# Kernel tuning notes

Measured on AMD Instinct MI355X. Metric: run time of the kernel, lower is better.

## Reference

```python
import jax, jax.numpy as jnp
import numpy as np

B = 2048        # batch
FEAT = 2048     # backbone feature dim (NIMA_attr stub input)
NUM_BINS = 9    # must match len(arange(1,5.5,0.5))
NUM_ATTR = 12
NUM_PT = 20
D = 64          # input_dim
H = 256         # hidden_size


def _mlp(x, W1, b1, W2, b2):
    return jax.nn.relu(x @ W1 + b1) @ W2 + b2


def _internal_interaction(e, W1, b1, W2, b2):
    # e: [B, A, D]; pairwise elementwise products -> tiny MLP -> sum over first attr axis
    pair = e[:, :, None, :] * e[:, None, :, :]          # [B, A, A, D]
    return _mlp(pair, W1, b1, W2, b2).sum(axis=1)       # [B, A, D]


def _gru_step(x, h, Wih, Whh, bih, bhh):
    # PyTorch GRUCell math; Wih/Whh stored as [D, 3D] with gate order r,z,n
    gi = x @ Wih + bih
    gh = h @ Whh + bhh
    ir, iz, inn = jnp.split(gi, 3, axis=-1)
    hr, hz, hn = jnp.split(gh, 3, axis=-1)
    r = jax.nn.sigmoid(ir + hr)
    z = jax.nn.sigmoid(iz + hz)
    n = jnp.tanh(inn + r * hn)
    return (1.0 - z) * n + z * h


def _interfuse(init, internal, external, Wih, Whh, bih, bhh):
    # so we batch the attribute dim and run the 3 sequential GRU steps once.
    h = _gru_step(init, jnp.zeros_like(init), Wih, Whh, bih, bhh)
    h = _gru_step(internal, h, Wih, Whh, bih, bhh)
    h = _gru_step(external, h, Wih, Whh, bih, bhh)
    return h


def setup_inputs() -> dict:
    key = jax.random.key(0)
    ks = jax.random.split(key, 40)
    def p(i, shape):
        return jax.random.normal(ks[i], shape, dtype=jnp.float32) * 0.05
    return dict(
        images=jax.random.normal(ks[0], (B, FEAT), dtype=jnp.float32),
        personal_traits=jax.random.normal(ks[1], (B, NUM_PT), dtype=jnp.float32),
        nima_Wl=p(2, (FEAT, NUM_BINS)), nima_bl=p(3, (NUM_BINS,)),
        nima_Wa=p(4, (FEAT, NUM_ATTR)), nima_ba=p(5, (NUM_ATTR,)),
        img_node_W1=p(6, (NUM_ATTR, H)), img_node_b1=p(7, (H,)),
        img_node_W2=p(8, (H, NUM_ATTR * D)), img_node_b2=p(9, (NUM_ATTR * D,)),
        user_node_W1=p(10, (NUM_PT, H)), user_node_b1=p(11, (H,)),
        user_node_W2=p(12, (H, NUM_ATTR * D)), user_node_b2=p(13, (NUM_ATTR * D,)),
        ii_img_W1=p(14, (D, H)), ii_img_b1=p(15, (H,)),
        ii_img_W2=p(16, (H, D)), ii_img_b2=p(17, (D,)),
        ii_user_W1=p(18, (D, H)), ii_user_b1=p(19, (H,)),
        ii_user_W2=p(20, (H, D)), ii_user_b2=p(21, (D,)),
        gru_img_Wih=p(22, (D, 3 * D)), gru_img_Whh=p(23, (D, 3 * D)),
        gru_img_bih=p(24, (3 * D,)), gru_img_bhh=p(25, (3 * D,)),
        gru_user_Wih=p(26, (D, 3 * D)), gru_user_Whh=p(27, (D, 3 * D)),
        gru_user_bih=p(28, (3 * D,)), gru_user_bhh=p(29, (3 * D,)),
        corr_W=p(30, (D, 1)), corr_b=p(31, (1,)),
        dist_W1=p(32, (NUM_BINS, H)), dist_b1=p(33, (H,)),
        dist_W2=p(34, (H, 1)), dist_b2=p(35, (1,)),
    )


def reference(images, personal_traits,
              nima_Wl, nima_bl, nima_Wa, nima_ba,
              img_node_W1, img_node_b1, img_node_W2, img_node_b2,
              user_node_W1, user_node_b1, user_node_W2, user_node_b2,
              ii_img_W1, ii_img_b1, ii_img_W2, ii_img_b2,
              ii_user_W1, ii_user_b1, ii_user_W2, ii_user_b2,
              gru_img_Wih, gru_img_Whh, gru_img_bih, gru_img_bhh,
              gru_user_Wih, gru_user_Whh, gru_user_bih, gru_user_bhh,
              corr_W, corr_b, dist_W1, dist_b1, dist_W2, dist_b2):
    # NIMA_attr stub: two linear heads on backbone features
    logit = images @ nima_Wl + nima_bl                       # [B, num_bins]
    attr_raw = images @ nima_Wa + nima_ba                    # [B, num_attr]

    attr_img = _mlp(attr_raw, img_node_W1, img_node_b1, img_node_W2, img_node_b2)
    attr_img = attr_img.reshape(-1, NUM_ATTR, D)
    attr_user = _mlp(personal_traits, user_node_W1, user_node_b1, user_node_W2, user_node_b2)
    attr_user = attr_user.reshape(-1, NUM_ATTR, D)

    prob = jax.nn.softmax(logit, axis=1)

    internal_img = _internal_interaction(attr_img, ii_img_W1, ii_img_b1, ii_img_W2, ii_img_b2)
    internal_user = _internal_interaction(attr_user, ii_user_W1, ii_user_b1, ii_user_W2, ii_user_b2)

    # ExternalInteraction: interaction[:,i,j] = user_i * img_j; sums factor out
    ext_user = attr_user * attr_img.sum(axis=1, keepdims=True)   # sum over j
    ext_img = attr_img * attr_user.sum(axis=1, keepdims=True)    # sum over i

    fused_img = _interfuse(attr_img, internal_img, ext_img,
                           gru_img_Wih, gru_img_Whh, gru_img_bih, gru_img_bhh)
    fused_user = _interfuse(attr_user, internal_user, ext_user,
                            gru_user_Wih, gru_user_Whh, gru_user_bih, gru_user_bhh)

    interaction_outputs = (fused_img.sum(axis=1) + fused_user.sum(axis=1)) @ corr_W + corr_b

    scale = jnp.arange(NUM_BINS, dtype=jnp.float32) * 0.5 + 1.0   # arange(1,5.5,0.5)
    direct_outputs = _mlp(prob * scale, dist_W1, dist_b1, dist_W2, dist_b2)
    return interaction_outputs + direct_outputs                  # [B, 1]
```

## Files before the change

kernel.cpp:

```cpp
#include <hip/hip_runtime.h>
#include <hip/hip_bf16.h>

#define NB 2048
#define FEAT 2048
#define NBINS 9
#define NATTR 12
#define NPT 20
#define DD 64
#define HH 256

typedef __attribute__((ext_vector_type(8))) short bf8v;
typedef __attribute__((ext_vector_type(4))) float f4v;
typedef __attribute__((ext_vector_type(16))) float f16v;

__device__ __forceinline__ unsigned short f2bf(float f) {
  unsigned int u = __float_as_uint(f);
  u += 0x7FFFu + ((u >> 16) & 1u);
  return (unsigned short)(u >> 16);
}

__device__ __forceinline__ unsigned int pkbf(float x, float y) {
  __hip_bfloat162 h = __float22bfloat162_rn(make_float2(x, y));
  union { __hip_bfloat162 h; unsigned int u; } cv;
  cv.h = h;
  return cv.u;
}

__global__ void k_prep_all(
    const float* __restrict__ Wl, const float* __restrict__ Wa,
    const float* __restrict__ Wih_i, const float* __restrict__ Whh_i,
    const float* __restrict__ Wih_u, const float* __restrict__ Whh_u,
    const float* __restrict__ W1i, const float* __restrict__ W1u,
    const float* __restrict__ W2i, const float* __restrict__ W2u,
    float* __restrict__ WT, unsigned short* __restrict__ WTg,
    unsigned short* __restrict__ W1T, unsigned short* __restrict__ W2T,
    float* __restrict__ outacc) {
  int bid = blockIdx.x, tid = threadIdx.x;
  if (bid < 168) {
    int idx = bid * 256 + tid;
    if (idx < 21 * FEAT) {
      int c = idx / FEAT, k = idx - c * FEAT;
      WT[idx] = (c < NBINS) ? Wl[k * NBINS + c] : Wa[k * NATTR + (c - NBINS)];
    }
  } else if (bid < 172) {
    if (tid < 192) {
      int idx = bid - 168;
      const float* W = idx == 0 ? Wih_i : idx == 1 ? Whh_i : idx == 2 ? Wih_u : Whh_u;
      unsigned short* dst = WTg + (size_t)idx * 192 * 72 + (size_t)tid * 72;
      for (int k = 0; k < DD; ++k) dst[k] = f2bf(W[k * 192 + tid]);
    }
  } else if (bid < 428) {
    int t = (bid - 172) * 256 + tid;
    if (t < 32768) {
      int dt = t >> 14, rem = t & 16383;
      int h = rem >> 6, k = rem & 63;
      W1T[t] = f2bf((dt ? W1u : W1i)[k * HH + h]);
    } else {
      int t2 = t - 32768;
      int dt = t2 >> 14, rem = t2 & 16383;
      int dp = rem >> 8, k = rem & 255;
      W2T[t2] = f2bf((dt ? W2u : W2i)[k * DD + dp]);
    }
  } else {
    int idx = (bid - 428) * 256 + tid;
    if (idx < NB) outacc[idx] = 0.f;
  }
}

__global__ __launch_bounds__(256) void k_nima(
    const float* __restrict__ A, const float* __restrict__ WT,
    const float* __restrict__ bl, const float* __restrict__ ba,
    const float* __restrict__ dW1, const float* __restrict__ db1,
    const float* __restrict__ dW2, const float* __restrict__ db2,
    float* __restrict__ attr_raw, float* __restrict__ direct) {
  int wave = threadIdx.x >> 6, lane = threadIdx.x & 63;
  int row = blockIdx.x * 4 + wave;
  const float4* A4 = (const float4*)(A + (size_t)row * FEAT);
  float acc[21];
#pragma unroll
  for (int c = 0; c < 21; ++c) acc[c] = 0.f;
#pragma unroll
  for (int it = 0; it < 8; ++it) {
    int kk = it * 64 + lane;
    float4 a = A4[kk];
#pragma unroll
    for (int c = 0; c < 21; ++c) {
      float4 w = ((const float4*)(WT + c * FEAT))[kk];
      acc[c] += a.x * w.x + a.y * w.y + a.z * w.z + a.w * w.w;
    }
  }
#pragma unroll
  for (int c = 0; c < 21; ++c) {
#pragma unroll
    for (int m = 1; m < 64; m <<= 1) acc[c] += __shfl_xor(acc[c], m);
  }
  if (lane == 0) {
#pragma unroll
    for (int c = 0; c < NATTR; ++c) attr_raw[row * NATTR + c] = acc[NBINS + c] + ba[c];
  }
  float l[NBINS];
  float mx = -1e30f;
#pragma unroll
  for (int i = 0; i < NBINS; ++i) { l[i] = acc[i] + bl[i]; mx = fmaxf(mx, l[i]); }
  float s = 0.f;
#pragma unroll
  for (int i = 0; i < NBINS; ++i) { l[i] = __expf(l[i] - mx); s += l[i]; }
  float inv = 1.f / s;
#pragma unroll
  for (int i = 0; i < NBINS; ++i) l[i] *= inv * (1.f + 0.5f * (float)i);
  float partial = 0.f;
#pragma unroll
  for (int hh = 0; hh < 4; ++hh) {
    int h = lane + hh * 64;
    float v = db1[h];
#pragma unroll
    for (int i = 0; i < NBINS; ++i) v += l[i] * dW1[i * HH + h];
    partial += fmaxf(v, 0.f) * dW2[h];
  }
#pragma unroll
  for (int m2 = 1; m2 < 64; m2 <<= 1) partial += __shfl_xor(partial, m2);
  if (lane == 0) direct[row] = partial + db2[0];
}

template <int DIN>
__device__ __forceinline__ void node_mlp_body(
    const float* __restrict__ X, const float* __restrict__ W1,
    const float* __restrict__ b1, const float* __restrict__ W2,
    const float* __restrict__ b2, float* __restrict__ out,
    float* __restrict__ cs, float* hlds, int r0) {
  int h = threadIdx.x;
  float w1r[DIN];
#pragma unroll
  for (int d = 0; d < DIN; ++d) w1r[d] = W1[d * HH + h];
  float b1h = b1[h];
#pragma unroll
  for (int r = 0; r < 8; ++r) {
    const float* x = X + (size_t)(r0 + r) * DIN;
    float s = b1h;
#pragma unroll
    for (int d = 0; d < DIN; ++d) s += x[d] * w1r[d];
    hlds[h * 8 + r] = fmaxf(s, 0.f);
  }
  __syncthreads();
  float acc[3][8];
#pragma unroll
  for (int oi = 0; oi < 3; ++oi)
#pragma unroll
    for (int r = 0; r < 8; ++r) acc[oi][r] = 0.f;
  for (int hh = 0; hh < HH; ++hh) {
    float4 a = ((const float4*)(hlds + hh * 8))[0];
    float4 bv = ((const float4*)(hlds + hh * 8))[1];
    float hv[8] = {a.x, a.y, a.z, a.w, bv.x, bv.y, bv.z, bv.w};
#pragma unroll
    for (int oi = 0; oi < 3; ++oi) {
      float w = W2[hh * 768 + threadIdx.x + oi * 256];
#pragma unroll
      for (int r = 0; r < 8; ++r) acc[oi][r] += hv[r] * w;
    }
  }
  float part[8];
#pragma unroll
  for (int r = 0; r < 8; ++r) part[r] = 0.f;
#pragma unroll
  for (int oi = 0; oi < 3; ++oi) {
    int o = threadIdx.x + oi * 256;
    float bb = b2[o];
#pragma unroll
    for (int r = 0; r < 8; ++r) {
      float val = acc[oi][r] + bb;
      out[(size_t)(r0 + r) * 768 + o] = val;
      part[r] += val;
    }
  }
  __syncthreads();
  {
    int w = threadIdx.x >> 6, d = threadIdx.x & 63;
#pragma unroll
    for (int r = 0; r < 8; ++r) hlds[(w * 8 + r) * 64 + d] = part[r];
  }
  __syncthreads();
#pragma unroll
  for (int rep = 0; rep < 2; ++rep) {
    int slot = threadIdx.x + rep * 256;
    int r = slot >> 6, d = slot & 63;
    cs[(size_t)(r0 + r) * DD + d] =
        hlds[(0 * 8 + r) * 64 + d] + hlds[(1 * 8 + r) * 64 + d] +
        hlds[(2 * 8 + r) * 64 + d] + hlds[(3 * 8 + r) * 64 + d];
  }
}

__global__ __launch_bounds__(256) void k_node_both(
    const float* __restrict__ attr_raw, const float* __restrict__ ptraits,
    const float* __restrict__ W1a, const float* __restrict__ b1a,
    const float* __restrict__ W2a, const float* __restrict__ b2a,
    const float* __restrict__ W1b, const float* __restrict__ b1b,
    const float* __restrict__ W2b, const float* __restrict__ b2b,
    float* __restrict__ attr_img, float* __restrict__ cs_img,
    float* __restrict__ attr_user, float* __restrict__ cs_user) {
  __shared__ __align__(16) float hlds[HH * 8];
  int r0 = blockIdx.x * 8;
  if (blockIdx.y == 0)
    node_mlp_body<NATTR>(attr_raw, W1a, b1a, W2a, b2a, attr_img, cs_img, hlds, r0);
  else
    node_mlp_body<NPT>(ptraits, W1b, b1b, W2b, b2b, attr_user, cs_user, hlds, r0);
}

__global__ __launch_bounds__(256, 4) void k_internal_mfma(
    const float* __restrict__ attr_img, const float* __restrict__ attr_user,
    const unsigned short* __restrict__ W1T, const unsigned short* __restrict__ W2T,
    const float* __restrict__ b1i, const float* __restrict__ b1u,
    const float* __restrict__ b2i, const float* __restrict__ b2u,
    float* __restrict__ int_img, float* __restrict__ int_user) {
  int b = blockIdx.x, dt = blockIdx.y;
  const float* e_g = (dt ? attr_user : attr_img) + (size_t)b * (NATTR * DD);
  const float* b1 = dt ? b1u : b1i;
  const float* b2 = dt ? b2u : b2i;
  float* outp = (dt ? int_user : int_img) + (size_t)b * (NATTR * DD);

  __shared__ __align__(16) float shQ[12 * 260];
  __shared__ __align__(16) unsigned short Plds[192 * 72];
  float* elds = shQ;

  int tid = threadIdx.x, w = tid >> 6, l = tid & 63;
  int l15 = l & 15, l4 = l >> 4, l31 = l & 31, hi = l >> 5;

  bf8v w1f[2][4];
#pragma unroll
  for (int nt = 0; nt < 2; ++nt)
#pragma unroll
    for (int ks = 0; ks < 4; ++ks)
      w1f[nt][ks] = *(const bf8v*)&W1T[(size_t)dt * 16384 +
                      (size_t)(w * 64 + nt * 32 + l31) * 64 + ks * 16 + hi * 8];
  bf8v w2f[8];
#pragma unroll
  for (int ks = 0; ks < 8; ++ks)
    w2f[ks] = *(const bf8v*)&W2T[(size_t)dt * 16384 +
                                 (size_t)(w * 16 + l15) * 256 + ks * 32 + l4 * 8];
  float b2v = b2[w * 16 + l15];
  float b1lo[2], b1hi_[2];
#pragma unroll
  for (int nt = 0; nt < 2; ++nt) {
    float v = b1[w * 64 + nt * 32 + l31];
    b1lo[nt] = v;
    b1hi_[nt] = hi ? -1e30f : v;
  }

  if (tid < 192) {
    int r = tid >> 4, c = tid & 15;
    *(float4*)&elds[r * 68 + c * 4] = ((const float4*)e_g)[tid];
  }
  __syncthreads();

#pragma unroll
  for (int rep = 0; rep < 3; ++rep) {
    int t2 = tid + rep * 256;
    int p = t2 >> 2, q4 = t2 & 3;
    int j = p >> 4, i = p & 15;
    unsigned int* dst = (unsigned int*)&Plds[p * 72 + q4 * 16];
    if (i < NATTR) {
      const float4* ei = (const float4*)(elds + i * 68 + q4 * 16);
      const float4* ej = (const float4*)(elds + j * 68 + q4 * 16);
      float4 a0 = ei[0], c0 = ej[0], a1 = ei[1], c1 = ej[1];
      float4 a2 = ei[2], c2 = ej[2], a3 = ei[3], c3 = ej[3];
      uint4 o0, o1;
      o0.x = pkbf(a0.x * c0.x, a0.y * c0.y); o0.y = pkbf(a0.z * c0.z, a0.w * c0.w);
      o0.z = pkbf(a1.x * c1.x, a1.y * c1.y); o0.w = pkbf(a1.z * c1.z, a1.w * c1.w);
      o1.x = pkbf(a2.x * c2.x, a2.y * c2.y); o1.y = pkbf(a2.z * c2.z, a2.w * c2.w);
      o1.z = pkbf(a3.x * c3.x, a3.y * c3.y); o1.w = pkbf(a3.z * c3.z, a3.w * c3.w);
      *(uint4*)dst = o0;
      *(uint4*)(dst + 4) = o1;
    } else {
      uint4 z = {0u, 0u, 0u, 0u};
      *(uint4*)dst = z;
      *(uint4*)(dst + 4) = z;
    }
  }
  __syncthreads();

#pragma unroll
  for (int m = 0; m < 6; ++m) {
    bf8v a[4];
#pragma unroll
    for (int ks = 0; ks < 4; ++ks)
      a[ks] = *(const bf8v*)&Plds[(m * 32 + l31) * 72 + ks * 16 + hi * 8];
#pragma unroll
    for (int nt = 0; nt < 2; ++nt) {
      f16v c = {0.f, 0.f, 0.f, 0.f, 0.f, 0.f, 0.f, 0.f,
                0.f, 0.f, 0.f, 0.f, 0.f, 0.f, 0.f, 0.f};
#pragma unroll
      for (int ks = 0; ks < 4; ++ks)
        c = __builtin_amdgcn_mfma_f32_32x32x16_bf16(a[ks], w1f[nt][ks], c, 0, 0, 0);
      float sA = 0.f, sB = 0.f;
#pragma unroll
      for (int r = 0; r < 8; ++r)
        sA += fmaxf(c[r] + (((r >> 2) & 1) ? b1hi_[nt] : b1lo[nt]), 0.f);
#pragma unroll
      for (int r = 8; r < 16; ++r)
        sB += fmaxf(c[r] + (((r >> 2) & 1) ? b1hi_[nt] : b1lo[nt]), 0.f);
      sA += __shfl_xor(sA, 32);
      sB += __shfl_xor(sB, 32);
      int col = w * 64 + nt * 32 + l31;
      if (hi == 0) shQ[(2 * m) * 260 + col] = sA;
      else         shQ[(2 * m + 1) * 260 + col] = sB;
    }
  }
  __syncthreads();

  f4v co = (f4v){0.f, 0.f, 0.f, 0.f};
#pragma unroll
  for (int ks = 0; ks < 8; ++ks) {
    union { bf8v v; uint4 u; } A;
    if (l15 < NATTR) {
      const float* qsrc = &shQ[l15 * 260 + ks * 32 + l4 * 8];
      float4 v0 = *(const float4*)qsrc;
      float4 v1 = *(const float4*)(qsrc + 4);
      A.u.x = pkbf(v0.x, v0.y); A.u.y = pkbf(v0.z, v0.w);
      A.u.z = pkbf(v1.x, v1.y); A.u.w = pkbf(v1.z, v1.w);
    } else {
      A.u = (uint4){0u, 0u, 0u, 0u};
    }
    co = __builtin_amdgcn_mfma_f32_16x16x32_bf16(A.v, w2f[ks], co, 0, 0, 0);
  }
#pragma unroll
  for (int r = 0; r < 4; ++r) {
    int j = l4 * 4 + r;
    if (j < NATTR) outp[j * DD + w * 16 + l15] = co[r] + 12.f * b2v;
  }
}

__global__ __launch_bounds__(256, 2) void k_gru_mfma(
    const float* __restrict__ attr_img, const float* __restrict__ attr_user,
    const float* __restrict__ int_img, const float* __restrict__ int_user,
    const float* __restrict__ cs_img, const float* __restrict__ cs_user,
    const unsigned short* __restrict__ WTg,
    const float* __restrict__ bih_i, const float* __restrict__ bhh_i,
    const float* __restrict__ bih_u, const float* __restrict__ bhh_u,
    const float* __restrict__ corr_W, float* __restrict__ outacc) {
  int blk = blockIdx.x, dt = blockIdx.y;
  int c0 = blk * 64;
  int tid = threadIdx.x, w = tid >> 6, l = tid & 63;
  int l15 = l & 15, l4 = l >> 4;

  const float* e   = (dt ? attr_user : attr_img);
  const float* itn = (dt ? int_user : int_img);
  const float* cs  = (dt ? cs_img : cs_user);
  const float* bih = (dt ? bih_u : bih_i);
  const float* bhh = (dt ? bhh_u : bhh_i);

  __shared__ __align__(16) unsigned short Wlds[2 * 192 * 72];
  __shared__ __align__(16) unsigned short Xb[64 * 72];
  __shared__ __align__(16) unsigned short Hb[64 * 72];

  {
    const unsigned short* src = WTg + (size_t)dt * (2 * 192 * 72);
    for (int v = tid; v < 3456; v += 256)
      *(bf8v*)&Wlds[v * 8] = *(const bf8v*)&src[v * 8];
  }
  float bihv[3][4], bhhv[3][4], cw[4];
#pragma unroll
  for (int t = 0; t < 3; ++t)
#pragma unroll
    for (int db = 0; db < 4; ++db) {
      bihv[t][db] = bih[t * 64 + db * 16 + l15];
      bhhv[t][db] = bhh[t * 64 + db * 16 + l15];
    }
#pragma unroll
  for (int db = 0; db < 4; ++db) cw[db] = corr_W[db * 16 + l15];

  float h_old[4][4];
#pragma unroll
  for (int db = 0; db < 4; ++db)
#pragma unroll
    for (int r = 0; r < 4; ++r) h_old[db][r] = 0.f;

  int row = tid >> 2;
  int chunk = tid & 3;
  size_t srcoff = (size_t)(c0 + row) * DD + chunk * 16;
  int bb_row = (c0 + row) / NATTR;

  __syncthreads();

#pragma unroll
  for (int step = 0; step < 3; ++step) {
    {
      const float* src = (step == 1 ? itn : e) + srcoff;
      float4 v0 = ((const float4*)src)[0];
      float4 v1 = ((const float4*)src)[1];
      float4 v2 = ((const float4*)src)[2];
      float4 v3 = ((const float4*)src)[3];
      if (step == 2) {
        const float4* c4 = (const float4*)(cs + (size_t)bb_row * DD + chunk * 16);
        float4 q0 = c4[0], q1 = c4[1], q2 = c4[2], q3 = c4[3];
        v0.x *= q0.x; v0.y *= q0.y; v0.z *= q0.z; v0.w *= q0.w;
        v1.x *= q1.x; v1.y *= q1.y; v1.z *= q1.z; v1.w *= q1.w;
        v2.x *= q2.x; v2.y *= q2.y; v2.z *= q2.z; v2.w *= q2.w;
        v3.x *= q3.x; v3.y *= q3.y; v3.z *= q3.z; v3.w *= q3.w;
      }
      uint4 o0, o1;
      o0.x = pkbf(v0.x, v0.y); o0.y = pkbf(v0.z, v0.w);
      o0.z = pkbf(v1.x, v1.y); o0.w = pkbf(v1.z, v1.w);
      o1.x = pkbf(v2.x, v2.y); o1.y = pkbf(v2.z, v2.w);
      o1.z = pkbf(v3.x, v3.y); o1.w = pkbf(v3.z, v3.w);
      unsigned int* dst = (unsigned int*)&Xb[row * 72 + chunk * 16];
      *(uint4*)dst = o0;
      *(uint4*)(dst + 4) = o1;
    }
    __syncthreads();

    f4v gi[3][4], gh[3][4];
#pragma unroll
    for (int t = 0; t < 3; ++t)
#pragma unroll
      for (int db = 0; db < 4; ++db) {
        gi[t][db] = (f4v){0.f, 0.f, 0.f, 0.f};
        gh[t][db] = (f4v){0.f, 0.f, 0.f, 0.f};
      }
#pragma unroll
    for (int ks = 0; ks < 2; ++ks) {
      bf8v ax = *(const bf8v*)&Xb[(w * 16 + l15) * 72 + ks * 32 + l4 * 8];
#pragma unroll
      for (int t = 0; t < 3; ++t)
#pragma unroll
        for (int db = 0; db < 4; ++db) {
          bf8v bw = *(const bf8v*)&Wlds[(t * 64 + db * 16 + l15) * 72 + ks * 32 + l4 * 8];
          gi[t][db] = __builtin_amdgcn_mfma_f32_16x16x32_bf16(ax, bw, gi[t][db], 0, 0, 0);
        }
      if (step > 0) {
        bf8v ah = *(const bf8v*)&Hb[(w * 16 + l15) * 72 + ks * 32 + l4 * 8];
#pragma unroll
        for (int t = 0; t < 3; ++t)
#pragma unroll
          for (int db = 0; db < 4; ++db) {
            bf8v bw = *(const bf8v*)&Wlds[(192 + t * 64 + db * 16 + l15) * 72 + ks * 32 + l4 * 8];
            gh[t][db] = __builtin_amdgcn_mfma_f32_16x16x32_bf16(ah, bw, gh[t][db], 0, 0, 0);
          }
      }
    }

#pragma unroll
    for (int db = 0; db < 4; ++db) {
#pragma unroll
      for (int r = 0; r < 4; ++r) {
        float ir = gi[0][db][r] + bihv[0][db];
        float hr = gh[0][db][r] + bhhv[0][db];
        float iz = gi[1][db][r] + bihv[1][db];
        float hz = gh[1][db][r] + bhhv[1][db];
        float in_ = gi[2][db][r] + bihv[2][db];
        float hn = gh[2][db][r] + bhhv[2][db];
        float rr = 1.f / (1.f + __expf(-(ir + hr)));
        float zz = 1.f / (1.f + __expf(-(iz + hz)));
        float ax_ = in_ + rr * hn;
        ax_ = fminf(fmaxf(ax_, -15.f), 15.f);
        float e2 = __expf(-2.f * ax_);
        float nn = (1.f - e2) / (1.f + e2);
        float h = (1.f - zz) * nn + zz * h_old[db][r];
        h_old[db][r] = h;
        if (step < 2)
          Hb[(w * 16 + l4 * 4 + r) * 72 + db * 16 + l15] = f2bf(h);
      }
    }
    __syncthreads();
  }

#pragma unroll
  for (int r = 0; r < 4; ++r) {
    float s = 0.f;
#pragma unroll
    for (int db = 0; db < 4; ++db) s += cw[db] * h_old[db][r];
#pragma unroll
    for (int m = 1; m < 16; m <<= 1) s += __shfl_xor(s, m);
    if (l15 == 0) {
      int chain = c0 + w * 16 + l4 * 4 + r;
      atomicAdd(&outacc[chain / NATTR], s);
    }
  }
}

__global__ void k_finalize(const float* __restrict__ outacc, const float* __restrict__ direct,
                           const float* __restrict__ corr_b, float* __restrict__ out) {
  int b = blockIdx.x * 256 + threadIdx.x;
  if (b < NB) out[b] = outacc[b] + direct[b] + corr_b[0];
}

extern "C" void kernel_launch(void* const* d_in, const int* in_sizes, int n_in,
                              void* d_out, int out_size, void* d_ws, size_t ws_size,
                              hipStream_t stream) {
  const float* images     = (const float*)d_in[0];
  const float* ptraits    = (const float*)d_in[1];
  const float* nima_Wl    = (const float*)d_in[2];
  const float* nima_bl    = (const float*)d_in[3];
  const float* nima_Wa    = (const float*)d_in[4];
  const float* nima_ba    = (const float*)d_in[5];
  const float* imgn_W1    = (const float*)d_in[6];
  const float* imgn_b1    = (const float*)d_in[7];
  const float* imgn_W2    = (const float*)d_in[8];
  const float* imgn_b2    = (const float*)d_in[9];
  const float* usrn_W1    = (const float*)d_in[10];
  const float* usrn_b1    = (const float*)d_in[11];
  const float* usrn_W2    = (const float*)d_in[12];
  const float* usrn_b2    = (const float*)d_in[13];
  const float* iiW1i      = (const float*)d_in[14];
  const float* iib1i      = (const float*)d_in[15];
  const float* iiW2i      = (const float*)d_in[16];
  const float* iib2i      = (const float*)d_in[17];
  const float* iiW1u      = (const float*)d_in[18];
  const float* iib1u      = (const float*)d_in[19];
  const float* iiW2u      = (const float*)d_in[20];
  const float* iib2u      = (const float*)d_in[21];
  const float* gWih_i     = (const float*)d_in[22];
  const float* gWhh_i     = (const float*)d_in[23];
  const float* gbih_i     = (const float*)d_in[24];
  const float* gbhh_i     = (const float*)d_in[25];
  const float* gWih_u     = (const float*)d_in[26];
  const float* gWhh_u     = (const float*)d_in[27];
  const float* gbih_u     = (const float*)d_in[28];
  const float* gbhh_u     = (const float*)d_in[29];
  const float* corr_W     = (const float*)d_in[30];
  const float* corr_b     = (const float*)d_in[31];
  const float* dist_W1    = (const float*)d_in[32];
  const float* dist_b1    = (const float*)d_in[33];
  const float* dist_W2    = (const float*)d_in[34];
  const float* dist_b2    = (const float*)d_in[35];

  float* ws = (float*)d_ws;
  float* WT        = ws;
  float* attr_raw  = WT + 21 * FEAT;
  float* attr_img  = attr_raw + NB * NATTR;
  float* attr_user = attr_img + NB * 768;
  float* int_img   = attr_user + NB * 768;
  float* int_user  = int_img + NB * 768;
  float* cs_img    = int_user + NB * 768;
  float* cs_user   = cs_img + NB * DD;
  float* direct    = cs_user + NB * DD;
  float* outacc    = direct + NB;
  unsigned short* WTg = (unsigned short*)(outacc + NB);
  unsigned short* W1T = WTg + 4 * 192 * 72;
  unsigned short* W2T = W1T + 2 * HH * DD;

  float* out = (float*)d_out;

  hipLaunchKernelGGL(k_prep_all, dim3(436), dim3(256), 0, stream,
                     nima_Wl, nima_Wa,
                     gWih_i, gWhh_i, gWih_u, gWhh_u,
                     iiW1i, iiW1u, iiW2i, iiW2u,
                     WT, WTg, W1T, W2T, outacc);
  hipLaunchKernelGGL(k_nima, dim3(NB / 4), dim3(256), 0, stream,
                     images, WT, nima_bl, nima_ba,
                     dist_W1, dist_b1, dist_W2, dist_b2,
                     attr_raw, direct);
  hipLaunchKernelGGL(k_node_both, dim3(NB / 8, 2), dim3(256), 0, stream,
                     attr_raw, ptraits,
                     imgn_W1, imgn_b1, imgn_W2, imgn_b2,
                     usrn_W1, usrn_b1, usrn_W2, usrn_b2,
                     attr_img, cs_img, attr_user, cs_user);
  hipLaunchKernelGGL(k_internal_mfma, dim3(NB, 2), dim3(256), 0, stream,
                     attr_img, attr_user, W1T, W2T,
                     iib1i, iib1u, iib2i, iib2u,
                     int_img, int_user);
  hipLaunchKernelGGL(k_gru_mfma, dim3(NB * NATTR / 64, 2), dim3(256), 0, stream,
                     attr_img, attr_user, int_img, int_user, cs_img, cs_user,
                     WTg, gbih_i, gbhh_i, gbih_u, gbhh_u, corr_W, outacc);
  hipLaunchKernelGGL(k_finalize, dim3(NB / 256), dim3(256), 0, stream,
                     outacc, direct, corr_b, out);
}
```

Before: 136.6 us.

## Move node MLP second layer to bf16 MFMA and fold internal bias into GEMM

The node-embedding MLP's second layer (256x768) now runs on bf16 MFMA 16x16x32 tiles over 16 rows per block, using a pre-transposed bf16 copy of W2 built in the prep kernel, in place of a scalar fp32 FMA loop. The internal-interaction kernel folds the first-layer bias into the GEMM by appending a ones column to the pair matrix and the bias row to W1. It also pads the K dimension to 80 and zero-fills the extra Q rows to drop the per-lane branches. This cuts VALU work and branching, but adds bf16 rounding in the node MLP, a fifth K-step of MFMA work, larger LDS padding, and a lower occupancy hint (4 to 3).

Result: no change. 137.8 us (+0.9%).

```diff
diff --git a/kernel.cpp b/kernel.cpp
--- a/kernel.cpp
+++ b/kernel.cpp
@@ -8,6 +8,7 @@
 #define NPT 20
 #define DD 64
 #define HH 256
+#define PST 88
 
 typedef __attribute__((ext_vector_type(8))) short bf8v;
 typedef __attribute__((ext_vector_type(4))) float f4v;
@@ -31,10 +32,12 @@
     const float* __restrict__ Wih_i, const float* __restrict__ Whh_i,
     const float* __restrict__ Wih_u, const float* __restrict__ Whh_u,
     const float* __restrict__ W1i, const float* __restrict__ W1u,
+    const float* __restrict__ b1i, const float* __restrict__ b1u,
     const float* __restrict__ W2i, const float* __restrict__ W2u,
+    const float* __restrict__ nW2i, const float* __restrict__ nW2u,
     float* __restrict__ WT, unsigned short* __restrict__ WTg,
-    unsigned short* __restrict__ W1T, unsigned short* __restrict__ W2T,
-    float* __restrict__ outacc) {
+    unsigned short* __restrict__ W1Tx, unsigned short* __restrict__ W2T,
+    unsigned short* __restrict__ W2Tn, float* __restrict__ outacc) {
   int bid = blockIdx.x, tid = threadIdx.x;
   if (bid < 168) {
     int idx = bid * 256 + tid;
@@ -49,20 +52,30 @@
       unsigned short* dst = WTg + (size_t)idx * 192 * 72 + (size_t)tid * 72;
       for (int k = 0; k < DD; ++k) dst[k] = f2bf(W[k * 192 + tid]);
     }
-  } else if (bid < 428) {
-    int t = (bid - 172) * 256 + tid;
-    if (t < 32768) {
-      int dt = t >> 14, rem = t & 16383;
-      int h = rem >> 6, k = rem & 63;
-      W1T[t] = f2bf((dt ? W1u : W1i)[k * HH + h]);
-    } else {
-      int t2 = t - 32768;
-      int dt = t2 >> 14, rem = t2 & 16383;
-      int dp = rem >> 8, k = rem & 255;
-      W2T[t2] = f2bf((dt ? W2u : W2i)[k * DD + dp]);
-    }
+  } else if (bid < 174) {
+    int dt = bid - 172;
+    const float* W1 = dt ? W1u : W1i;
+    const float* b1 = dt ? b1u : b1i;
+    unsigned short* dst = W1Tx + (size_t)dt * (HH * 80) + (size_t)tid * 80;
+    for (int k = 0; k < DD; ++k) dst[k] = f2bf(W1[k * HH + tid]);
+    dst[64] = f2bf(b1[tid]);
+    for (int k = 65; k < 80; ++k) dst[k] = 0;
+  } else if (bid < 302) {
+    int t = (bid - 174) * 256 + tid;
+    int dt = t >> 14, rem = t & 16383;
+    int dp = rem >> 8, k = rem & 255;
+    W2T[t] = f2bf((dt ? W2u : W2i)[k * DD + dp]);
+  } else if (bid < 494) {
+    int idx8 = (bid - 302) * 256 + tid;
+    int dt = idx8 >= 24576;
+    int rem = idx8 - dt * 24576;
+    int o = rem >> 5, kb = (rem & 31) * 8;
+    const float* W2n = dt ? nW2u : nW2i;
+    unsigned short* dst = W2Tn + (size_t)idx8 * 8;
+#pragma unroll
+    for (int e = 0; e < 8; ++e) dst[e] = f2bf(W2n[(size_t)(kb + e) * 768 + o]);
   } else {
-    int idx = (bid - 428) * 256 + tid;
+    int idx = (bid - 494) * 256 + tid;
     if (idx < NB) outacc[idx] = 0.f;
   }
 }
@@ -125,153 +138,153 @@
 template <int DIN>
 __device__ __forceinline__ void node_mlp_body(
     const float* __restrict__ X, const float* __restrict__ W1,
-    const float* __restrict__ b1, const float* __restrict__ W2,
+    const float* __restrict__ b1, const unsigned short* __restrict__ W2Tn,
     const float* __restrict__ b2, float* __restrict__ out,
-    float* __restrict__ cs, float* hlds, int r0) {
-  int h = threadIdx.x;
-  float w1r[DIN];
-#pragma unroll
-  for (int d = 0; d < DIN; ++d) w1r[d] = W1[d * HH + h];
-  float b1h = b1[h];
-#pragma unroll
-  for (int r = 0; r < 8; ++r) {
-    const float* x = X + (size_t)(r0 + r) * DIN;
-    float s = b1h;
-#pragma unroll
-    for (int d = 0; d < DIN; ++d) s += x[d] * w1r[d];
-    hlds[h * 8 + r] = fmaxf(s, 0.f);
+    float* __restrict__ cs, unsigned short* hbf, float* cspart, int r0) {
+  int tid = threadIdx.x;
+  int w = tid >> 6, l = tid & 63, l15 = l & 15, l4 = l >> 4;
+  {
+    float w1r[DIN];
+#pragma unroll
+    for (int d = 0; d < DIN; ++d) w1r[d] = W1[d * HH + tid];
+    float b1h = b1[tid];
+#pragma unroll
+    for (int r = 0; r < 16; ++r) {
+      const float* x = X + (size_t)(r0 + r) * DIN;
+      float s = b1h;
+#pragma unroll
+      for (int d = 0; d < DIN; ++d) s += x[d] * w1r[d];
+      hbf[r * 264 + tid] = f2bf(fmaxf(s, 0.f));
+    }
   }
   __syncthreads();
-  float acc[3][8];
-#pragma unroll
-  for (int oi = 0; oi < 3; ++oi)
-#pragma unroll
-    for (int r = 0; r < 8; ++r) acc[oi][r] = 0.f;
-  for (int hh = 0; hh < HH; ++hh) {
-    float4 a = ((const float4*)(hlds + hh * 8))[0];
-    float4 bv = ((const float4*)(hlds + hh * 8))[1];
-    float hv[8] = {a.x, a.y, a.z, a.w, bv.x, bv.y, bv.z, bv.w};
-#pragma unroll
-    for (int oi = 0; oi < 3; ++oi) {
-      float w = W2[hh * 768 + threadIdx.x + oi * 256];
-#pragma unroll
-      for (int r = 0; r < 8; ++r) acc[oi][r] += hv[r] * w;
-    }
-  }
-  float part[8];
-#pragma unroll
-  for (int r = 0; r < 8; ++r) part[r] = 0.f;
-#pragma unroll
-  for (int oi = 0; oi < 3; ++oi) {
-    int o = threadIdx.x + oi * 256;
-    float bb = b2[o];
-#pragma unroll
-    for (int r = 0; r < 8; ++r) {
-      float val = acc[oi][r] + bb;
-      out[(size_t)(r0 + r) * 768 + o] = val;
-      part[r] += val;
-    }
-  }
+  bf8v a[8];
+#pragma unroll
+  for (int ks = 0; ks < 8; ++ks)
+    a[ks] = *(const bf8v*)&hbf[l15 * 264 + ks * 32 + l4 * 8];
+  float dsum[4][4];
+#pragma unroll
+  for (int q = 0; q < 4; ++q)
+#pragma unroll
+    for (int r = 0; r < 4; ++r) dsum[q][r] = 0.f;
+#pragma unroll
+  for (int nt = 0; nt < 12; ++nt) {
+    int col = w * 192 + nt * 16 + l15;
+    f4v c = (f4v){0.f, 0.f, 0.f, 0.f};
+#pragma unroll
+    for (int ks = 0; ks < 8; ++ks) {
+      bf8v bfr = *(const bf8v*)&W2Tn[(size_t)col * 256 + ks * 32 + l4 * 8];
+      c = __builtin_amdgcn_mfma_f32_16x16x32_bf16(a[ks], bfr, c, 0, 0, 0);
+    }
+    float bb = b2[col];
+#pragma unroll
+    for (int r = 0; r < 4; ++r) {
+      float v = c[r] + bb;
+      out[(size_t)(r0 + l4 * 4 + r) * 768 + col] = v;
+      dsum[nt & 3][r] += v;
+    }
+  }
+#pragma unroll
+  for (int q = 0; q < 4; ++q)
+#pragma unroll
+    for (int r = 0; r < 4; ++r)
+      cspart[(w * 16 + l4 * 4 + r) * 64 + q * 16 + l15] = dsum[q][r];
   __syncthreads();
-  {
-    int w = threadIdx.x >> 6, d = threadIdx.x & 63;
-#pragma unroll
-    for (int r = 0; r < 8; ++r) hlds[(w * 8 + r) * 64 + d] = part[r];
-  }
-  __syncthreads();
-#pragma unroll
-  for (int rep = 0; rep < 2; ++rep) {
-    int slot = threadIdx.x + rep * 256;
-    int r = slot >> 6, d = slot & 63;
-    cs[(size_t)(r0 + r) * DD + d] =
-        hlds[(0 * 8 + r) * 64 + d] + hlds[(1 * 8 + r) * 64 + d] +
-        hlds[(2 * 8 + r) * 64 + d] + hlds[(3 * 8 + r) * 64 + d];
+#pragma unroll
+  for (int rep = 0; rep < 4; ++rep) {
+    int slot = tid + rep * 256;
+    int row = slot >> 6, d = slot & 63;
+    cs[(size_t)(r0 + row) * DD + d] =
+        cspart[(0 * 16 + row) * 64 + d] + cspart[(1 * 16 + row) * 64 + d] +
+        cspart[(2 * 16 + row) * 64 + d] + cspart[(3 * 16 + row) * 64 + d];
   }
 }
 
 __global__ __launch_bounds__(256) void k_node_both(
     const float* __restrict__ attr_raw, const float* __restrict__ ptraits,
-    const float* __restrict__ W1a, const float* __restrict__ b1a,
-    const float* __restrict__ W2a, const float* __restrict__ b2a,
-    const float* __restrict__ W1b, const float* __restrict__ b1b,
-    const float* __restrict__ W2b, const float* __restrict__ b2b,
+    const float* __restrict__ W1a, const float* __restrict__ b1a, const float* __restrict__ b2a,
+    const float* __restrict__ W1b, const float* __restrict__ b1b, const float* __restrict__ b2b,
+    const unsigned short* __restrict__ W2Tn,
     float* __restrict__ attr_img, float* __restrict__ cs_img,
     float* __restrict__ attr_user, float* __restrict__ cs_user) {
-  __shared__ __align__(16) float hlds[HH * 8];
-  int r0 = blockIdx.x * 8;
+  __shared__ __align__(16) unsigned short hbf[16 * 264];
+  __shared__ __align__(16) float cspart[4 * 16 * 64];
+  int r0 = blockIdx.x * 16;
   if (blockIdx.y == 0)
-    node_mlp_body<NATTR>(attr_raw, W1a, b1a, W2a, b2a, attr_img, cs_img, hlds, r0);
+    node_mlp_body<NATTR>(attr_raw, W1a, b1a, W2Tn, b2a, attr_img, cs_img, hbf, cspart, r0);
   else
-    node_mlp_body<NPT>(ptraits, W1b, b1b, W2b, b2b, attr_user, cs_user, hlds, r0);
-}
-
-__global__ __launch_bounds__(256, 4) void k_internal_mfma(
+    node_mlp_body<NPT>(ptraits, W1b, b1b, W2Tn + (size_t)768 * 256, b2b,
+                       attr_user, cs_user, hbf, cspart, r0);
+}
+
+__global__ __launch_bounds__(256, 3) void k_internal_mfma(
     const float* __restrict__ attr_img, const float* __restrict__ attr_user,
-    const unsigned short* __restrict__ W1T, const unsigned short* __restrict__ W2T,
-    const float* __restrict__ b1i, const float* __restrict__ b1u,
+    const unsigned short* __restrict__ W1Tx, const unsigned short* __restrict__ W2T,
     const float* __restrict__ b2i, const float* __restrict__ b2u,
     float* __restrict__ int_img, float* __restrict__ int_user) {
   int b = blockIdx.x, dt = blockIdx.y;
   const float* e_g = (dt ? attr_user : attr_img) + (size_t)b * (NATTR * DD);
-  const float* b1 = dt ? b1u : b1i;
   const float* b2 = dt ? b2u : b2i;
   float* outp = (dt ? int_user : int_img) + (size_t)b * (NATTR * DD);
 
-  __shared__ __align__(16) float shQ[12 * 260];
-  __shared__ __align__(16) unsigned short Plds[192 * 72];
+  __shared__ __align__(16) float shQ[16 * 260];
+  __shared__ __align__(16) unsigned short Plds[192 * PST];
   float* elds = shQ;
 
   int tid = threadIdx.x, w = tid >> 6, l = tid & 63;
   int l15 = l & 15, l4 = l >> 4, l31 = l & 31, hi = l >> 5;
 
-  bf8v w1f[2][4];
+  bf8v w1f[2][5];
 #pragma unroll
   for (int nt = 0; nt < 2; ++nt)
 #pragma unroll
-    for (int ks = 0; ks < 4; ++ks)
-      w1f[nt][ks] = *(const bf8v*)&W1T[(size_t)dt * 16384 +
-                      (size_t)(w * 64 + nt * 32 + l31) * 64 + ks * 16 + hi * 8];
+    for (int ks = 0; ks < 5; ++ks)
+      w1f[nt][ks] = *(const bf8v*)&W1Tx[(size_t)dt * (HH * 80) +
+                      (size_t)(w * 64 + nt * 32 + l31) * 80 + ks * 16 + hi * 8];
   bf8v w2f[8];
 #pragma unroll
   for (int ks = 0; ks < 8; ++ks)
     w2f[ks] = *(const bf8v*)&W2T[(size_t)dt * 16384 +
                                  (size_t)(w * 16 + l15) * 256 + ks * 32 + l4 * 8];
   float b2v = b2[w * 16 + l15];
-  float b1lo[2], b1hi_[2];
-#pragma unroll
-  for (int nt = 0; nt < 2; ++nt) {
-    float v = b1[w * 64 + nt * 32 + l31];
-    b1lo[nt] = v;
-    b1hi_[nt] = hi ? -1e30f : v;
-  }
 
   if (tid < 192) {
     int r = tid >> 4, c = tid & 15;
     *(float4*)&elds[r * 68 + c * 4] = ((const float4*)e_g)[tid];
   }
+  for (int z = tid; z < 4 * 260; z += 256) shQ[12 * 260 + z] = 0.f;
   __syncthreads();
 
 #pragma unroll
-  for (int rep = 0; rep < 3; ++rep) {
+  for (int rep = 0; rep < 4; ++rep) {
     int t2 = tid + rep * 256;
-    int p = t2 >> 2, q4 = t2 & 3;
-    int j = p >> 4, i = p & 15;
-    unsigned int* dst = (unsigned int*)&Plds[p * 72 + q4 * 16];
-    if (i < NATTR) {
-      const float4* ei = (const float4*)(elds + i * 68 + q4 * 16);
-      const float4* ej = (const float4*)(elds + j * 68 + q4 * 16);
-      float4 a0 = ei[0], c0 = ej[0], a1 = ei[1], c1 = ej[1];
-      float4 a2 = ei[2], c2 = ej[2], a3 = ei[3], c3 = ej[3];
-      uint4 o0, o1;
-      o0.x = pkbf(a0.x * c0.x, a0.y * c0.y); o0.y = pkbf(a0.z * c0.z, a0.w * c0.w);
-      o0.z = pkbf(a1.x * c1.x, a1.y * c1.y); o0.w = pkbf(a1.z * c1.z, a1.w * c1.w);
-      o1.x = pkbf(a2.x * c2.x, a2.y * c2.y); o1.y = pkbf(a2.z * c2.z, a2.w * c2.w);
-      o1.z = pkbf(a3.x * c3.x, a3.y * c3.y); o1.w = pkbf(a3.z * c3.z, a3.w * c3.w);
-      *(uint4*)dst = o0;
-      *(uint4*)(dst + 4) = o1;
-    } else {
+    if (t2 < 768) {
+      int p = t2 >> 2, q4 = t2 & 3;
+      int j = p >> 4, i = p & 15;
+      unsigned int* dst = (unsigned int*)&Plds[p * PST + q4 * 16];
+      if (i < NATTR) {
+        const float4* ei = (const float4*)(elds + i * 68 + q4 * 16);
+        const float4* ej = (const float4*)(elds + j * 68 + q4 * 16);
+        float4 a0 = ei[0], c0 = ej[0], a1 = ei[1], c1 = ej[1];
+        float4 a2 = ei[2], c2 = ej[2], a3 = ei[3], c3 = ej[3];
+        uint4 o0, o1;
+        o0.x = pkbf(a0.x * c0.x, a0.y * c0.y); o0.y = pkbf(a0.z * c0.z, a0.w * c0.w);
+        o0.z = pkbf(a1.x * c1.x, a1.y * c1.y); o0.w = pkbf(a1.z * c1.z, a1.w * c1.w);
+        o1.x = pkbf(a2.x * c2.x, a2.y * c2.y); o1.y = pkbf(a2.z * c2.z, a2.w * c2.w);
+        o1.z = pkbf(a3.x * c3.x, a3.y * c3.y); o1.w = pkbf(a3.z * c3.z, a3.w * c3.w);
+        *(uint4*)dst = o0;
+        *(uint4*)(dst + 4) = o1;
+      } else {
+        uint4 z = {0u, 0u, 0u, 0u};
+        *(uint4*)dst = z;
+        *(uint4*)(dst + 4) = z;
+      }
+    } else if (t2 < 960) {
+      int p = t2 - 768;
+      unsigned int* dst = (unsigned int*)&Plds[p * PST + 64];
+      uint4 first = {((p & 15) < NATTR) ? 0x00003F80u : 0u, 0u, 0u, 0u};
       uint4 z = {0u, 0u, 0u, 0u};
-      *(uint4*)dst = z;
+      *(uint4*)dst = first;
       *(uint4*)(dst + 4) = z;
     }
   }
@@ -279,24 +292,22 @@
 
 #pragma unroll
   for (int m = 0; m < 6; ++m) {
-    bf8v a[4];
-#pragma unroll
-    for (int ks = 0; ks < 4; ++ks)
-      a[ks] = *(const bf8v*)&Plds[(m * 32 + l31) * 72 + ks * 16 + hi * 8];
+    bf8v a[5];
+#pragma unroll
+    for (int ks = 0; ks < 5; ++ks)
+      a[ks] = *(const bf8v*)&Plds[(m * 32 + l31) * PST + ks * 16 + hi * 8];
 #pragma unroll
     for (int nt = 0; nt < 2; ++nt) {
       f16v c = {0.f, 0.f, 0.f, 0.f, 0.f, 0.f, 0.f, 0.f,
                 0.f, 0.f, 0.f, 0.f, 0.f, 0.f, 0.f, 0.f};
 #pragma unroll
-      for (int ks = 0; ks < 4; ++ks)
+      for (int ks = 0; ks < 5; ++ks)
         c = __builtin_amdgcn_mfma_f32_32x32x16_bf16(a[ks], w1f[nt][ks], c, 0, 0, 0);
       float sA = 0.f, sB = 0.f;
 #pragma unroll
-      for (int r = 0; r < 8; ++r)
-        sA += fmaxf(c[r] + (((r >> 2) & 1) ? b1hi_[nt] : b1lo[nt]), 0.f);
-#pragma unroll
-      for (int r = 8; r < 16; ++r)
-        sB += fmaxf(c[r] + (((r >> 2) & 1) ? b1hi_[nt] : b1lo[nt]), 0.f);
+      for (int r = 0; r < 8; ++r) sA += fmaxf(c[r], 0.f);
+#pragma unroll
+      for (int r = 8; r < 16; ++r) sB += fmaxf(c[r], 0.f);
       sA += __shfl_xor(sA, 32);
       sB += __shfl_xor(sB, 32);
       int col = w * 64 + nt * 32 + l31;
@@ -310,15 +321,11 @@
 #pragma unroll
   for (int ks = 0; ks < 8; ++ks) {
     union { bf8v v; uint4 u; } A;
-    if (l15 < NATTR) {
-      const float* qsrc = &shQ[l15 * 260 + ks * 32 + l4 * 8];
-      float4 v0 = *(const float4*)qsrc;
-      float4 v1 = *(const float4*)(qsrc + 4);
-      A.u.x = pkbf(v0.x, v0.y); A.u.y = pkbf(v0.z, v0.w);
-      A.u.z = pkbf(v1.x, v1.y); A.u.w = pkbf(v1.z, v1.w);
-    } else {
-      A.u = (uint4){0u, 0u, 0u, 0u};
-    }
+    const float* qsrc = &shQ[l15 * 260 + ks * 32 + l4 * 8];
+    float4 v0 = *(const float4*)qsrc;
+    float4 v1 = *(const float4*)(qsrc + 4);
+    A.u.x = pkbf(v0.x, v0.y); A.u.y = pkbf(v0.z, v0.w);
+    A.u.z = pkbf(v1.x, v1.y); A.u.w = pkbf(v1.z, v1.w);
     co = __builtin_amdgcn_mfma_f32_16x16x32_bf16(A.v, w2f[ks], co, 0, 0, 0);
   }
 #pragma unroll
@@ -533,29 +540,32 @@
   float* cs_user   = cs_img + NB * DD;
   float* direct    = cs_user + NB * DD;
   float* outacc    = direct + NB;
-  unsigned short* WTg = (unsigned short*)(outacc + NB);
-  unsigned short* W1T = WTg + 4 * 192 * 72;
-  unsigned short* W2T = W1T + 2 * HH * DD;
+  unsigned short* WTg  = (unsigned short*)(outacc + NB);
+  unsigned short* W1Tx = WTg + 4 * 192 * 72;
+  unsigned short* W2T  = W1Tx + 2 * HH * 80;
+  unsigned short* W2Tn = W2T + 2 * DD * HH;
 
   float* out = (float*)d_out;
 
-  hipLaunchKernelGGL(k_prep_all, dim3(436), dim3(256), 0, stream,
+  hipLaunchKernelGGL(k_prep_all, dim3(502), dim3(256), 0, stream,
                      nima_Wl, nima_Wa,
                      gWih_i, gWhh_i, gWih_u, gWhh_u,
-                     iiW1i, iiW1u, iiW2i, iiW2u,
-                     WT, WTg, W1T, W2T, outacc);
+                     iiW1i, iiW1u, iib1i, iib1u, iiW2i, iiW2u,
+                     imgn_W2, usrn_W2,
+                     WT, WTg, W1Tx, W2T, W2Tn, outacc);
   hipLaunchKernelGGL(k_nima, dim3(NB / 4), dim3(256), 0, stream,
                      images, WT, nima_bl, nima_ba,
                      dist_W1, dist_b1, dist_W2, dist_b2,
                      attr_raw, direct);
-  hipLaunchKernelGGL(k_node_both, dim3(NB / 8, 2), dim3(256), 0, stream,
+  hipLaunchKernelGGL(k_node_both, dim3(NB / 16, 2), dim3(256), 0, stream,
                      attr_raw, ptraits,
-                     imgn_W1, imgn_b1, imgn_W2, imgn_b2,
-                     usrn_W1, usrn_b1, usrn_W2, usrn_b2,
+                     imgn_W1, imgn_b1, imgn_b2,
+                     usrn_W1, usrn_b1, usrn_b2,
+                     W2Tn,
                      attr_img, cs_img, attr_user, cs_user);
   hipLaunchKernelGGL(k_internal_mfma, dim3(NB, 2), dim3(256), 0, stream,
-                     attr_img, attr_user, W1T, W2T,
-                     iib1i, iib1u, iib2i, iib2u,
+                     attr_img, attr_user, W1Tx, W2T,
+                     iib2i, iib2u,
                      int_img, int_user);
   hipLaunchKernelGGL(k_gru_mfma, dim3(NB * NATTR / 64, 2), dim3(256), 0, stream,
                      attr_img, attr_user, int_img, int_user, cs_img, cs_user,
```
